# Kernel tuning notes

Hardware: AMD Instinct MI355X
Metric: run time of the kernel (lower is better)

Reference implementation:

```python
import jax, jax.numpy as jnp
import numpy as np

TEMP_LEN = 16
TARGET_LEN = 22
DIM = 768
HEADS = 12
B = 16
NT = TEMP_LEN * TEMP_LEN          # 256 template tokens
NG = TARGET_LEN * TARGET_LEN      # 484 target tokens
N = NT + NG                       # 740
POS_HID = 512


def _gaussian_heatmap(center, size, sig=1.0):
    x_axis = np.linspace(0, size[0] - 1, size[0]) - center[0]
    y_axis = np.linspace(0, size[1] - 1, size[1]) - center[1]
    xx, yy = np.meshgrid(x_axis, y_axis)
    return np.exp(-0.5 * (xx ** 2 + yy ** 2) / sig ** 2)


def _bias_index(L):
    # faithful to getBiasIndex (w_len == h_len here)
    coords = np.stack(np.meshgrid(np.arange(L), np.arange(L), indexing='ij'))  # [2,L,L]
    flat = coords.reshape(2, -1)                                               # [2,L*L]
    rel = (flat[:, :, None] - flat[:, None, :]).transpose(1, 2, 0).astype(np.int64)
    rel[:, :, 0] += L - 1
    rel[:, :, 1] += L - 1
    rel[:, :, 0] *= 2 * L - 1
    return rel.sum(-1)  # [L*L, L*L]


def setup_inputs() -> dict:
    key = jax.random.key(0)
    ks = jax.random.split(key, 12)
    f32 = jnp.float32
    x = jax.random.normal(ks[0], (B, N, DIM), dtype=f32)
    temp_q = jax.random.normal(ks[1], (B, NT, DIM), dtype=f32)
    target_q = jax.random.normal(ks[2], (B, NG, DIM), dtype=f32)
    # linear weights stored [in, out] (transposed torch layout)
    w = lambda k, i, o: jax.random.normal(k, (i, o), dtype=f32) * 0.02
    q_w = w(ks[3], DIM, DIM)
    k_w = w(ks[4], DIM, DIM)
    v_w = w(ks[5], DIM, DIM)
    proj_w = w(ks[6], DIM, DIM)
    proj_b = jnp.zeros((DIM,), dtype=f32)
    rpb_table = jax.random.normal(ks[7], ((2 * TARGET_LEN - 1) ** 2, HEADS), dtype=f32) * 0.0002
    rpb_table_temp = jax.random.normal(ks[8], ((2 * TEMP_LEN - 1) ** 2, HEADS), dtype=f32) * 0.0002
    pos_w1 = w(ks[9], 2, POS_HID)
    pos_b1 = jnp.zeros((POS_HID,), dtype=f32)
    pos_w2 = w(ks[10], POS_HID, HEADS)
    pos_b2 = jnp.zeros((HEADS,), dtype=f32)
    # deterministic cross-bias coordinate table (non-learned buffer)
    temp_tab = _gaussian_heatmap((TEMP_LEN // 2, TEMP_LEN // 2), (TEMP_LEN, TEMP_LEN)).astype(np.float32).flatten() \
        + np.linspace(-0.2, 0.2, NT, dtype=np.float32)
    targ_tab = _gaussian_heatmap((TARGET_LEN // 2, TARGET_LEN // 2), (TARGET_LEN, TARGET_LEN)).astype(np.float32).flatten() \
        + np.linspace(-0.2, 0.2, NG, dtype=np.float32)
    # torch.meshgrid default indexing='ij': [2, NT, NG] -> permute(1,2,0) -> [NT,NG,2]
    temp_target = np.stack(np.meshgrid(temp_tab, targ_tab, indexing='ij')).transpose(1, 2, 0)
    target_temp_tab = jnp.asarray(temp_target.transpose(1, 0, 2))  # [NG, NT, 2]
    temp_idx = jnp.asarray(_bias_index(TEMP_LEN))       # [NT, NT] int64
    target_idx = jnp.asarray(_bias_index(TARGET_LEN))   # [NG, NG] int64
    return {
        'x': x, 'temp_q': temp_q, 'target_q': target_q,
        'q_w': q_w, 'k_w': k_w, 'v_w': v_w, 'proj_w': proj_w, 'proj_b': proj_b,
        'rpb_table': rpb_table, 'rpb_table_temp': rpb_table_temp,
        'pos_w1': pos_w1, 'pos_b1': pos_b1, 'pos_w2': pos_w2, 'pos_b2': pos_b2,
        'target_temp_tab': target_temp_tab,
        'temp_idx': temp_idx, 'target_idx': target_idx,
    }


def reference(x, temp_q, target_q, q_w, k_w, v_w, proj_w, proj_b,
              rpb_table, rpb_table_temp, pos_w1, pos_b1, pos_w2, pos_b2,
              target_temp_tab, temp_idx, target_idx):
    Bsz, Ntok, C = x.shape
    H = HEADS
    hd = C // H
    scale = hd ** -0.5

    q_in = jnp.concatenate([temp_q, target_q], axis=1)                 # [B,N,C]
    q = (q_in @ q_w).reshape(Bsz, Ntok, H, hd).transpose(0, 2, 1, 3)   # [B,H,N,hd]
    k = (x @ k_w).reshape(Bsz, Ntok, H, hd).transpose(0, 2, 1, 3)
    v = (x @ v_w).reshape(Bsz, Ntok, H, hd).transpose(0, 2, 1, 3)

    # gathered relative position biases -> [H, Ni, Ni]
    temp_rpb = rpb_table_temp[temp_idx.reshape(-1)].reshape(NT, NT, H).transpose(2, 0, 1)
    targ_rpb = rpb_table[target_idx.reshape(-1)].reshape(NG, NG, H).transpose(2, 0, 1)
    # MLP cross bias: [NG, NT, 2] -> [NG, NT, H] -> [H, NG, NT]
    hid = jax.nn.relu(target_temp_tab @ pos_w1 + pos_b1)
    target_temp_bias = (hid @ pos_w2 + pos_b2).transpose(2, 0, 1)      # [H,NG,NT]
    temp_target_bias = target_temp_bias.transpose(0, 2, 1)             # [H,NT,NG]
    top = jnp.concatenate([temp_rpb, temp_target_bias], axis=2)        # [H,NT,N]
    bot = jnp.concatenate([target_temp_bias, targ_rpb], axis=2)        # [H,NG,N]
    bias = jnp.concatenate([top, bot], axis=1)[None]                   # [1,H,N,N]

    attn = jnp.einsum('bhnd,bhmd->bhnm', q, k) * scale + bias
    attn = jax.nn.softmax(attn, axis=-1)
    out = jnp.einsum('bhnm,bhmd->bhnd', attn, v).transpose(0, 2, 1, 3).reshape(Bsz, Ntok, C)
    return out @ proj_w + proj_b
```

## Files before the change

### kernel.cpp

```cpp
#include <hip/hip_runtime.h>


typedef unsigned short u16;
typedef short bf16x8 __attribute__((ext_vector_type(8)));
typedef float f32x4 __attribute__((ext_vector_type(4)));

#define BSZ   16
#define NTOK  740
#define NTMP  256
#define NTGT  484
#define DIMC  768
#define NHEAD 12
#define HDIM  64
#define MROWS (BSZ*NTOK)
#define LOG2E 1.44269504f
#define NEGS  (-23.0831032f)

__device__ __forceinline__ float bflo(unsigned int u) {
    return __uint_as_float(u << 16);
}
__device__ __forceinline__ float bfhi(unsigned int u) {
    return __uint_as_float(u & 0xffff0000u);
}
__device__ __forceinline__ u16 f2bf(float f) {
    unsigned int u = __float_as_uint(f);
    u += 0x7fffu + ((u >> 16) & 1u);
    return (u16)(u >> 16);
}

__device__ __forceinline__ void gl_lds16(const u16* g, u16* l) {
    __builtin_amdgcn_global_load_lds(
        (const __attribute__((address_space(1))) unsigned int*)(unsigned long long)g,
        (__attribute__((address_space(3))) unsigned int*)(unsigned int)(unsigned long long)l,
        16, 0, 0);
}

__device__ __forceinline__ size_t b2off(int h, int i, int j) {
    return ((size_t)(h * NTOK + i)) * 768 + ((j >> 6) << 6) + ((j & 15) << 2) + ((j >> 4) & 3);
}

#define PREP_MLP  484
#define PREP_TRW  (PREP_MLP + 576)
#define PREP_ALL  (PREP_TRW + 2220)

__global__ __launch_bounds__(256) void prep_kernel(
    const float* __restrict__ w0, const float* __restrict__ w1,
    const float* __restrict__ w2, const float* __restrict__ w3,
    u16* __restrict__ Wt,
    const float* __restrict__ rpb, const float* __restrict__ rpbt,
    const int* __restrict__ tidx, const int* __restrict__ gidx,
    const float* __restrict__ pw1, const float* __restrict__ pb1,
    const float* __restrict__ pw2, const float* __restrict__ pb2,
    const float* __restrict__ tab, u16* __restrict__ bias)
{
    __shared__ float T[64][65];
    const int blk = blockIdx.x;
    const int tid = threadIdx.x;

    if (blk < PREP_MLP) {
        int g = blk;
        int t = tid;
        float a  = tab[(g * NTMP + t) * 2 + 0];
        float bb = tab[(g * NTMP + t) * 2 + 1];
        float acc[NHEAD];
        #pragma unroll
        for (int h = 0; h < NHEAD; h++) acc[h] = pb2[h];
        for (int k = 0; k < 512; k++) {
            float hid = fmaxf(a * pw1[k] + bb * pw1[512 + k] + pb1[k], 0.0f);
            #pragma unroll
            for (int h = 0; h < NHEAD; h++) acc[h] += hid * pw2[k * NHEAD + h];
        }
        #pragma unroll
        for (int h = 0; h < NHEAD; h++) {
            u16 v = f2bf(acc[h] * LOG2E);
            bias[b2off(h, t, NTMP + g)] = v;
            bias[b2off(h, NTMP + g, t)] = v;
        }
    } else if (blk < PREP_TRW) {
        int t = blk - PREP_MLP;
        int z = t / 144, rem = t - z * 144;
        int bx = rem % 12, by = rem / 12;
        const float* src = (z == 0) ? w0 : (z == 1) ? w1 : (z == 2) ? w2 : w3;
        const float scale = (z == 0) ? 0.125f * LOG2E : 1.0f;
        u16* dst = Wt + (size_t)z * DIMC * DIMC;
        int out0 = bx * 64, in0 = by * 64;
        #pragma unroll
        for (int l = 0; l < 4; l++) {
            int u = tid + (l << 8);
            int r = u >> 4, c4 = (u & 15) << 2;
            float4 p = *(const float4*)(src + (size_t)(in0 + r) * DIMC + out0 + c4);
            T[r][c4] = p.x; T[r][c4 + 1] = p.y; T[r][c4 + 2] = p.z; T[r][c4 + 3] = p.w;
        }
        __syncthreads();
        #pragma unroll
        for (int l = 0; l < 2; l++) {
            int u = tid + (l << 8);
            int r = u >> 3, c8 = (u & 7) << 3;
            u16 e[8];
            #pragma unroll
            for (int i = 0; i < 8; i++) e[i] = f2bf(T[c8 + i][r] * scale);
            *(uint4*)(dst + (size_t)(out0 + r) * DIMC + in0 + c8) = *(uint4*)e;
        }
    } else {
        int t = blk - PREP_TRW;
        int jb = t % 3, i = t / 3;
        int j = jb * 256 + tid;
        u16 vals[NHEAD];
        if (j >= NTOK) {
            u16 neg = f2bf(-1e30f);
            #pragma unroll
            for (int h = 0; h < NHEAD; h++) vals[h] = neg;
        } else if (i < NTMP && j < NTMP) {
            int idx = tidx[i * NTMP + j];
            #pragma unroll
            for (int h = 0; h < NHEAD; h++) vals[h] = f2bf(rpbt[idx * NHEAD + h] * LOG2E);
        } else if (i >= NTMP && j >= NTMP) {
            int idx = gidx[(i - NTMP) * NTGT + (j - NTMP)];
            #pragma unroll
            for (int h = 0; h < NHEAD; h++) vals[h] = f2bf(rpb[idx * NHEAD + h] * LOG2E);
        } else {
            return;
        }
        #pragma unroll
        for (int h = 0; h < NHEAD; h++) bias[b2off(h, i, j)] = vals[h];
    }
}

__global__ __launch_bounds__(256, 6) void gemm_qkv(
    const float* __restrict__ x, const float* __restrict__ tq,
    const float* __restrict__ gq, const u16* __restrict__ Wt,
    u16* __restrict__ Qo, u16* __restrict__ Ko, u16* __restrict__ Vo)
{
    __shared__ __align__(16) u16 As[4096];
    __shared__ __align__(16) u16 Bs[8192];
    const int tid = threadIdx.x;
    const int lane = tid & 63, w = tid >> 6;
    const int quad = lane >> 4, ln = lane & 15;

    const int nwg = 18 * 185;
    const int flat = blockIdx.y * 18 + blockIdx.x;
    const int q = nwg >> 3, r = nwg & 7;
    const int xcd = flat & 7, sidx = flat >> 3;
    const int wg = (xcd < r) ? xcd * (q + 1) + sidx
                             : r * (q + 1) + (xcd - r) * q + sidx;
    const int by = wg / 18, bx = wg - by * 18;

    const int m0 = by << 6;
    const int wm = (w >> 1) << 5, wn = (w & 1) << 6;

    const int p = (bx < 6) ? 0 : (bx < 12) ? 1 : 2;
    const int nn = (bx - p * 6) << 7;
    const u16* Wb = Wt + (size_t)p * DIMC * DIMC + (size_t)nn * DIMC;
    u16* Co = (p == 0) ? Qo : (p == 1) ? Ko : Vo;

    const int rr = tid >> 2, qq = tid & 3;
    const int arow = m0 + rr;
    const float* aptr;
    if (p == 0) {
        int b = arow / NTOK, n = arow - b * NTOK;
        aptr = (n < NTMP)
             ? tq + ((size_t)(b * NTMP + n)) * DIMC
             : gq + ((size_t)(b * NTGT + (n - NTMP))) * DIMC;
    } else {
        aptr = x + (size_t)arow * DIMC;
    }
    const int wof0 = ((2 * qq + 0) * 64 + (rr ^ (2 * qq + 0))) * 8;
    const int wof1 = ((2 * qq + 1) * 64 + (rr ^ (2 * qq + 1))) * 8;

    f32x4 acc[2][4];
    #pragma unroll
    for (int i = 0; i < 2; i++)
        #pragma unroll
        for (int j = 0; j < 4; j++) acc[i][j] = (f32x4){0.f, 0.f, 0.f, 0.f};

    #pragma unroll 1
    for (int t = 0; t < 12; t++) {
        const int k0 = t << 6;
        __syncthreads();
        const float* s = aptr + k0 + (qq << 4);
        float4 a0 = ((const float4*)s)[0], a1 = ((const float4*)s)[1];
        float4 a2 = ((const float4*)s)[2], a3 = ((const float4*)s)[3];
        #pragma unroll
        for (int l = 0; l < 4; l++) {
            int f = tid + (l << 8);
            int c8 = f >> 7, r2 = f & 127;
            gl_lds16(Wb + (size_t)r2 * DIMC + k0 + c8 * 8, &Bs[f * 8]);
        }
        u16 e[16] = {f2bf(a0.x), f2bf(a0.y), f2bf(a0.z), f2bf(a0.w),
                     f2bf(a1.x), f2bf(a1.y), f2bf(a1.z), f2bf(a1.w),
                     f2bf(a2.x), f2bf(a2.y), f2bf(a2.z), f2bf(a2.w),
                     f2bf(a3.x), f2bf(a3.y), f2bf(a3.z), f2bf(a3.w)};
        *(uint4*)&As[wof0] = ((uint4*)e)[0];
        *(uint4*)&As[wof1] = ((uint4*)e)[1];
        __syncthreads();
        #pragma unroll
        for (int kp = 0; kp < 2; kp++) {
            const int kc0 = (kp << 2) + quad;
            bf16x8 af[2], bfr[4];
            #pragma unroll
            for (int mt = 0; mt < 2; mt++)
                af[mt] = *(const bf16x8*)
                    &As[(kc0 * 64 + wm + mt * 16 + (ln ^ kc0)) * 8];
            #pragma unroll
            for (int nt = 0; nt < 4; nt++)
                bfr[nt] = *(const bf16x8*)
                    &Bs[(kc0 * 128 + wn + nt * 16 + ln) * 8];
            #pragma unroll
            for (int mt = 0; mt < 2; mt++)
                #pragma unroll
                for (int nt = 0; nt < 4; nt++)
                    acc[mt][nt] = __builtin_amdgcn_mfma_f32_16x16x32_bf16(
                        af[mt], bfr[nt], acc[mt][nt], 0, 0, 0);
        }
    }

    #pragma unroll
    for (int mt = 0; mt < 2; mt++)
        #pragma unroll
        for (int reg = 0; reg < 4; reg++) {
            int grow = m0 + wm + mt * 16 + (quad << 2) + reg;
            #pragma unroll
            for (int nt = 0; nt < 4; nt++)
                Co[(size_t)grow * DIMC + nn + wn + nt * 16 + ln]
                    = f2bf(acc[mt][nt][reg]);
        }
}

__global__ __launch_bounds__(256) void gemm_proj(
    const u16* __restrict__ A, const u16* __restrict__ Wt,
    const float* __restrict__ pb, float* __restrict__ Cf)
{
    __shared__ __align__(16) u16 As[4096];
    __shared__ __align__(16) u16 Bs[8192];
    const int tid = threadIdx.x;
    const int lane = tid & 63, w = tid >> 6;
    const int quad = lane >> 4, ln = lane & 15;

    const int nwg = 6 * 185;
    const int flat = blockIdx.y * 6 + blockIdx.x;
    const int q = nwg >> 3, r = nwg & 7;
    const int xcd = flat & 7, sidx = flat >> 3;
    const int wg = (xcd < r) ? xcd * (q + 1) + sidx
                             : r * (q + 1) + (xcd - r) * q + sidx;
    const int by = wg / 6, bx = wg - by * 6;

    const int m0 = by << 6;
    const int wm = (w >> 1) << 5, wn = (w & 1) << 6;
    const int nn = bx << 7;
    const u16* Wb = Wt + (size_t)nn * DIMC;

    f32x4 acc[2][4];
    #pragma unroll
    for (int i = 0; i < 2; i++)
        #pragma unroll
        for (int j = 0; j < 4; j++) acc[i][j] = (f32x4){0.f, 0.f, 0.f, 0.f};

    #pragma unroll 1
    for (int t = 0; t < 12; t++) {
        __syncthreads();
        const int k0 = t << 6;
        #pragma unroll
        for (int l = 0; l < 2; l++) {
            int f = tid + (l << 8);
            int c8 = f >> 6, r2 = f & 63;
            gl_lds16(A + (size_t)(m0 + r2) * DIMC + k0 + c8 * 8, &As[f * 8]);
        }
        #pragma unroll
        for (int l = 0; l < 4; l++) {
            int f = tid + (l << 8);
            int c8 = f >> 7, r2 = f & 127;
            gl_lds16(Wb + (size_t)r2 * DIMC + k0 + c8 * 8, &Bs[f * 8]);
        }
        __syncthreads();
        #pragma unroll
        for (int kp = 0; kp < 2; kp++) {
            bf16x8 af[2], bfr[4];
            #pragma unroll
            for (int mt = 0; mt < 2; mt++)
                af[mt] = *(const bf16x8*)
                    &As[(((kp << 2) + quad) * 64 + wm + mt * 16 + ln) * 8];
            #pragma unroll
            for (int nt = 0; nt < 4; nt++)
                bfr[nt] = *(const bf16x8*)
                    &Bs[(((kp << 2) + quad) * 128 + wn + nt * 16 + ln) * 8];
            #pragma unroll
            for (int mt = 0; mt < 2; mt++)
                #pragma unroll
                for (int nt = 0; nt < 4; nt++)
                    acc[mt][nt] = __builtin_amdgcn_mfma_f32_16x16x32_bf16(
                        af[mt], bfr[nt], acc[mt][nt], 0, 0, 0);
        }
    }

    #pragma unroll
    for (int mt = 0; mt < 2; mt++)
        #pragma unroll
        for (int reg = 0; reg < 4; reg++) {
            int grow = m0 + wm + mt * 16 + (quad << 2) + reg;
            #pragma unroll
            for (int nt = 0; nt < 4; nt++) {
                int gcol = nn + wn + nt * 16 + ln;
                Cf[(size_t)grow * DIMC + gcol] = acc[mt][nt][reg] + pb[gcol];
            }
        }
}

__global__ __launch_bounds__(256) void attn_mfma(
    const u16* __restrict__ Qg, const u16* __restrict__ Kg,
    const u16* __restrict__ Vg, const u16* __restrict__ bias,
    u16* __restrict__ ctx)
{
    __shared__ __align__(16) u16 KsL[4096];
    __shared__ __align__(16) u16 VtL[64 * 72];
    __shared__ __align__(16) u16 Pw[4][16][72];

    const int tid = threadIdx.x;
    const int lane = tid & 63, w = tid >> 6;
    const int quad = lane >> 4, ln = lane & 15;

    const int flat = (blockIdx.z * 12 + blockIdx.y) * 12 + blockIdx.x;
    const int wg = (flat & 7) * 288 + (flat >> 3);
    const int h = wg / 192;
    const int rem = wg - h * 192;
    const int b = rem / 12;
    const int q0 = (rem - b * 12) << 6;

    const int mbase = q0 + (w << 4);
    const u16* bp = bias + ((size_t)h * NTOK) * 768;

    bf16x8 aq[2];
    {
        int qrow = mbase + ln; if (qrow >= NTOK) qrow = NTOK - 1;
        #pragma unroll
        for (int kp = 0; kp < 2; kp++)
            aq[kp] = *(const bf16x8*)(Qg + ((size_t)(b * NTOK + qrow)) * DIMC
                                      + h * HDIM + kp * 32 + (quad << 3));
    }
    int boff[4];
    #pragma unroll
    for (int reg = 0; reg < 4; reg++) {
        int rr = mbase + (quad << 2) + reg;
        if (rr >= NTOK) rr = NTOK - 1;
        boff[reg] = rr * 768 + (ln << 2);
    }

    const int pswz = ((ln >> 2) & 3) << 4;

    float rs[4] = {};
    f32x4 O[4];
    #pragma unroll
    for (int dt = 0; dt < 4; dt++) O[dt] = (f32x4){0.f, 0.f, 0.f, 0.f};

    for (int j0 = 0; j0 < NTOK; j0 += 64) {
        __syncthreads();
        #pragma unroll
        for (int l = 0; l < 2; l++) {
            int f = tid + (l << 8);
            int chunk = f >> 6, jr = f & 63;
            int krow = j0 + jr; if (krow >= NTOK) krow = NTOK - 1;
            gl_lds16(Kg + ((size_t)(b * NTOK + krow)) * DIMC + h * HDIM + chunk * 8,
                     KsL + f * 8);
        }
        uint2 bvv[4];
        #pragma unroll
        for (int reg = 0; reg < 4; reg++)
            bvv[reg] = *(const uint2*)(bp + boff[reg] + j0);
        #pragma unroll
        for (int l = 0; l < 2; l++) {
            int u = tid + (l << 8);
            int jr = u >> 3, d0 = (u & 7) << 3;
            int vrow = j0 + jr; if (vrow >= NTOK) vrow = NTOK - 1;
            uint4 p = *(const uint4*)(Vg + ((size_t)(b * NTOK + vrow)) * DIMC + h * HDIM + d0);
            const u16* pe = (const u16*)&p;
            int jswz = jr ^ d0;
            #pragma unroll
            for (int i = 0; i < 8; i++) VtL[(d0 + i) * 72 + jswz] = pe[i];
        }
        __syncthreads();

        bf16x8 bv[4][2];
        #pragma unroll
        for (int dt = 0; dt < 4; dt++) {
            int key8 = ((dt * 2 + (ln >> 3)) & 7) << 3;
            #pragma unroll
            for (int kp = 0; kp < 2; kp++) {
                int koff = (kp * 32 + (quad << 3)) ^ key8;
                bv[dt][kp] = *(const bf16x8*)&VtL[(dt * 16 + ln) * 72 + koff];
            }
        }

        f32x4 s[4];
        #pragma unroll
        for (int nt = 0; nt < 4; nt++) s[nt] = (f32x4){NEGS, NEGS, NEGS, NEGS};
        __builtin_amdgcn_s_setprio(1);
        #pragma unroll
        for (int kp = 0; kp < 2; kp++)
            #pragma unroll
            for (int nt = 0; nt < 4; nt++) {
                bf16x8 bk = *(const bf16x8*)
                    &KsL[(((kp << 2) + quad) * 64 + nt * 16 + ln) * 8];
                s[nt] = __builtin_amdgcn_mfma_f32_16x16x32_bf16(aq[kp], bk, s[nt], 0, 0, 0);
            }
        __builtin_amdgcn_s_setprio(0);

        #pragma unroll
        for (int reg = 0; reg < 4; reg++) {
            uint2 bb = bvv[reg];
            float p0 = __builtin_exp2f(s[0][reg] + bflo(bb.x));
            float p1 = __builtin_exp2f(s[1][reg] + bfhi(bb.x));
            float p2 = __builtin_exp2f(s[2][reg] + bflo(bb.y));
            float p3 = __builtin_exp2f(s[3][reg] + bfhi(bb.y));
            s[0][reg] = p0; s[1][reg] = p1;
            s[2][reg] = p2; s[3][reg] = p3;
            rs[reg] += p0 + p1 + p2 + p3;
        }
        u16* pwb = &Pw[w][0][0];
        #pragma unroll
        for (int nt = 0; nt < 4; nt++) {
            int colw = ((nt ^ quad) << 4) + ln;
            #pragma unroll
            for (int reg = 0; reg < 4; reg++)
                pwb[((quad << 2) + reg) * 72 + colw] = f2bf(s[nt][reg]);
        }
        bf16x8 ap[2];
        #pragma unroll
        for (int kp = 0; kp < 2; kp++) {
            int koff = (kp * 32 + (quad << 3)) ^ pswz;
            ap[kp] = *(const bf16x8*)&pwb[ln * 72 + koff];
        }
        __builtin_amdgcn_s_setprio(1);
        #pragma unroll
        for (int dt = 0; dt < 4; dt++)
            #pragma unroll
            for (int kp = 0; kp < 2; kp++)
                O[dt] = __builtin_amdgcn_mfma_f32_16x16x32_bf16(
                    ap[kp], bv[dt][kp], O[dt], 0, 0, 0);
        __builtin_amdgcn_s_setprio(0);
    }

    #pragma unroll
    for (int reg = 0; reg < 4; reg++) {
        float t = rs[reg];
        #pragma unroll
        for (int mk = 8; mk >= 1; mk >>= 1) t += __shfl_xor(t, mk);
        float inv = 1.0f / t;
        int row = mbase + (quad << 2) + reg;
        if (row < NTOK) {
            #pragma unroll
            for (int dt = 0; dt < 4; dt++)
                ctx[((size_t)(b * NTOK + row)) * DIMC + h * HDIM + dt * 16 + ln]
                    = f2bf(O[dt][reg] * inv);
        }
    }
}

extern "C" void kernel_launch(void* const* d_in, const int* in_sizes, int n_in,
                              void* d_out, int out_size, void* d_ws, size_t ws_size,
                              hipStream_t stream)
{
    const float* x        = (const float*)d_in[0];
    const float* temp_q   = (const float*)d_in[1];
    const float* target_q = (const float*)d_in[2];
    const float* q_w      = (const float*)d_in[3];
    const float* k_w      = (const float*)d_in[4];
    const float* v_w      = (const float*)d_in[5];
    const float* proj_w   = (const float*)d_in[6];
    const float* proj_b   = (const float*)d_in[7];
    const float* rpb      = (const float*)d_in[8];
    const float* rpbt     = (const float*)d_in[9];
    const float* pw1      = (const float*)d_in[10];
    const float* pb1      = (const float*)d_in[11];
    const float* pw2      = (const float*)d_in[12];
    const float* pb2      = (const float*)d_in[13];
    const float* tab      = (const float*)d_in[14];
    const int*   tidx     = (const int*)d_in[15];
    const int*   gidx     = (const int*)d_in[16];
    float* out = (float*)d_out;

    char* ws = (char*)d_ws;
    const size_t S = (size_t)MROWS * DIMC * sizeof(u16);
    const size_t SZB = (size_t)NHEAD * NTOK * 768 * sizeof(u16);
    u16* CTX   = (u16*)(ws);
    u16* V     = (u16*)(ws + S);
    u16* Q     = (u16*)(ws + 2 * S);
    u16* K     = (u16*)(ws + 3 * S);
    u16* BIAS2 = (u16*)(ws + 4 * S);
    u16* WT    = (u16*)(ws + 4 * S + SZB);

    prep_kernel<<<dim3(PREP_ALL), 256, 0, stream>>>(
        q_w, k_w, v_w, proj_w, WT,
        rpb, rpbt, tidx, gidx,
        pw1, pb1, pw2, pb2, tab, BIAS2);

    const u16* WTp = WT + 3 * (size_t)DIMC * DIMC;

    gemm_qkv<<<dim3(18, 185), 256, 0, stream>>>(x, temp_q, target_q, WT, Q, K, V);
    attn_mfma<<<dim3(12, 12, 16), 256, 0, stream>>>(Q, K, V, BIAS2, CTX);
    gemm_proj<<<dim3(6, 185), 256, 0, stream>>>(CTX, WTp, proj_b, out);
}
```

Measured before the change: 470.7 us.

## Keep A rows resident in QKV GEMM and double-buffer attention K/V/bias loads

The QKV GEMM now runs one 512-thread block per 64-row strip (Q strip or shared K/V strip). Each block converts the full fp32 A rows to bf16 into LDS once and loops over all output column tiles, with a double-buffered weight stage. This removes the repeated fp32 A reads and bf16 conversions across the 18 column blocks. In exchange, only 370 large blocks are launched, with heavy LDS use and uneven work between Q and K/V blocks, so occupancy and load balance may suffer. The attention kernel also double-buffers K in LDS and prefetches the next V and bias tiles into registers to overlap global loads with MFMA work.

```diff
diff --git a/kernel.cpp b/kernel.cpp
--- a/kernel.cpp
+++ b/kernel.cpp
@@ -126,104 +126,124 @@
     }
 }
 
-__global__ __launch_bounds__(256, 6) void gemm_qkv(
+__global__ __launch_bounds__(512) void gemm_qkv(
     const float* __restrict__ x, const float* __restrict__ tq,
     const float* __restrict__ gq, const u16* __restrict__ Wt,
     u16* __restrict__ Qo, u16* __restrict__ Ko, u16* __restrict__ Vo)
 {
-    __shared__ __align__(16) u16 As[4096];
-    __shared__ __align__(16) u16 Bs[8192];
+    __shared__ __align__(16) u16 As[96 * 64 * 8];
+    __shared__ __align__(16) u16 Bs[2][8192];
     const int tid = threadIdx.x;
     const int lane = tid & 63, w = tid >> 6;
     const int quad = lane >> 4, ln = lane & 15;
 
-    const int nwg = 18 * 185;
-    const int flat = blockIdx.y * 18 + blockIdx.x;
+    const int nwg = 370;
+    const int flat = blockIdx.x;
     const int q = nwg >> 3, r = nwg & 7;
     const int xcd = flat & 7, sidx = flat >> 3;
     const int wg = (xcd < r) ? xcd * (q + 1) + sidx
                              : r * (q + 1) + (xcd - r) * q + sidx;
-    const int by = wg / 18, bx = wg - by * 18;
-
+    const int kvtype = (wg >= 185) ? 1 : 0;
+    const int by = kvtype ? (wg - 185) : wg;
     const int m0 = by << 6;
-    const int wm = (w >> 1) << 5, wn = (w & 1) << 6;
-
-    const int p = (bx < 6) ? 0 : (bx < 12) ? 1 : 2;
-    const int nn = (bx - p * 6) << 7;
-    const u16* Wb = Wt + (size_t)p * DIMC * DIMC + (size_t)nn * DIMC;
-    u16* Co = (p == 0) ? Qo : (p == 1) ? Ko : Vo;
-
-    const int rr = tid >> 2, qq = tid & 3;
+
+    const int wm = (w >> 2) << 5;
+    const int wn = (w & 3) << 5;
+
+    const int rr = tid >> 3, qe = tid & 7;
     const int arow = m0 + rr;
     const float* aptr;
-    if (p == 0) {
+    if (!kvtype) {
         int b = arow / NTOK, n = arow - b * NTOK;
-        aptr = (n < NTMP)
-             ? tq + ((size_t)(b * NTMP + n)) * DIMC
-             : gq + ((size_t)(b * NTGT + (n - NTMP))) * DIMC;
+        aptr = (n < NTMP) ? tq + ((size_t)(b * NTMP + n)) * DIMC
+                          : gq + ((size_t)(b * NTGT + (n - NTMP))) * DIMC;
     } else {
         aptr = x + (size_t)arow * DIMC;
     }
-    const int wof0 = ((2 * qq + 0) * 64 + (rr ^ (2 * qq + 0))) * 8;
-    const int wof1 = ((2 * qq + 1) * 64 + (rr ^ (2 * qq + 1))) * 8;
-
-    f32x4 acc[2][4];
-    #pragma unroll
-    for (int i = 0; i < 2; i++)
-        #pragma unroll
-        for (int j = 0; j < 4; j++) acc[i][j] = (f32x4){0.f, 0.f, 0.f, 0.f};
-
-    #pragma unroll 1
-    for (int t = 0; t < 12; t++) {
-        const int k0 = t << 6;
-        __syncthreads();
-        const float* s = aptr + k0 + (qq << 4);
+    #pragma unroll
+    for (int j = 0; j < 12; j++) {
+        const float* s = aptr + j * 64 + qe * 8;
         float4 a0 = ((const float4*)s)[0], a1 = ((const float4*)s)[1];
-        float4 a2 = ((const float4*)s)[2], a3 = ((const float4*)s)[3];
-        #pragma unroll
-        for (int l = 0; l < 4; l++) {
-            int f = tid + (l << 8);
-            int c8 = f >> 7, r2 = f & 127;
-            gl_lds16(Wb + (size_t)r2 * DIMC + k0 + c8 * 8, &Bs[f * 8]);
-        }
-        u16 e[16] = {f2bf(a0.x), f2bf(a0.y), f2bf(a0.z), f2bf(a0.w),
-                     f2bf(a1.x), f2bf(a1.y), f2bf(a1.z), f2bf(a1.w),
-                     f2bf(a2.x), f2bf(a2.y), f2bf(a2.z), f2bf(a2.w),
-                     f2bf(a3.x), f2bf(a3.y), f2bf(a3.z), f2bf(a3.w)};
-        *(uint4*)&As[wof0] = ((uint4*)e)[0];
-        *(uint4*)&As[wof1] = ((uint4*)e)[1];
-        __syncthreads();
-        #pragma unroll
-        for (int kp = 0; kp < 2; kp++) {
-            const int kc0 = (kp << 2) + quad;
-            bf16x8 af[2], bfr[4];
-            #pragma unroll
-            for (int mt = 0; mt < 2; mt++)
-                af[mt] = *(const bf16x8*)
-                    &As[(kc0 * 64 + wm + mt * 16 + (ln ^ kc0)) * 8];
-            #pragma unroll
-            for (int nt = 0; nt < 4; nt++)
-                bfr[nt] = *(const bf16x8*)
-                    &Bs[(kc0 * 128 + wn + nt * 16 + ln) * 8];
-            #pragma unroll
-            for (int mt = 0; mt < 2; mt++)
+        u16 e[8] = {f2bf(a0.x), f2bf(a0.y), f2bf(a0.z), f2bf(a0.w),
+                    f2bf(a1.x), f2bf(a1.y), f2bf(a1.z), f2bf(a1.w)};
+        *(uint4*)&As[((j * 8 + qe) * 64 + (rr ^ qe)) * 8] = *(uint4*)e;
+    }
+
+#define WB_OF(pi) ((!kvtype) ? (Wt + ((size_t)(pi) << 7) * DIMC)                          \
+                 : ((pi) < 6) ? (Wt + (size_t)DIMC * DIMC + ((size_t)(pi) << 7) * DIMC)   \
+                              : (Wt + 2 * (size_t)DIMC * DIMC + ((size_t)((pi) - 6) << 7) * DIMC))
+
+#define STAGEB(Wb, t, s) do {                                                 \
+    _Pragma("unroll")                                                         \
+    for (int l = 0; l < 2; l++) {                                             \
+        int f = tid + (l << 9);                                               \
+        int c8 = f >> 7, r2 = f & 127;                                        \
+        gl_lds16((Wb) + (size_t)r2 * DIMC + ((t) << 6) + c8 * 8,              \
+                 &Bs[s][f * 8]);                                              \
+    } } while (0)
+
+    const int NP = kvtype ? 12 : 6;
+    STAGEB(WB_OF(0), 0, 0);
+    __syncthreads();
+
+    int buf = 0;
+    for (int pi = 0; pi < NP; pi++) {
+        const u16* WbC = WB_OF(pi);
+        const u16* WbN = (pi + 1 < NP) ? WB_OF(pi + 1) : WbC;
+        f32x4 acc[2][2];
+        #pragma unroll
+        for (int i = 0; i < 2; i++)
+            #pragma unroll
+            for (int j = 0; j < 2; j++) acc[i][j] = (f32x4){0.f, 0.f, 0.f, 0.f};
+
+        #pragma unroll 1
+        for (int t = 0; t < 12; t++) {
+            if (!((pi == NP - 1) && (t == 11))) {
+                const u16* Ws = (t < 11) ? WbC : WbN;
+                int tn = (t < 11) ? (t + 1) : 0;
+                STAGEB(Ws, tn, buf ^ 1);
+            }
+            #pragma unroll
+            for (int kp = 0; kp < 2; kp++) {
+                const int key = (kp << 2) + quad;
+                const int C = (t << 3) + key;
+                bf16x8 af[2], bfr[2];
                 #pragma unroll
-                for (int nt = 0; nt < 4; nt++)
-                    acc[mt][nt] = __builtin_amdgcn_mfma_f32_16x16x32_bf16(
-                        af[mt], bfr[nt], acc[mt][nt], 0, 0, 0);
-        }
-    }
-
-    #pragma unroll
-    for (int mt = 0; mt < 2; mt++)
-        #pragma unroll
-        for (int reg = 0; reg < 4; reg++) {
-            int grow = m0 + wm + mt * 16 + (quad << 2) + reg;
-            #pragma unroll
-            for (int nt = 0; nt < 4; nt++)
-                Co[(size_t)grow * DIMC + nn + wn + nt * 16 + ln]
-                    = f2bf(acc[mt][nt][reg]);
-        }
+                for (int mt = 0; mt < 2; mt++)
+                    af[mt] = *(const bf16x8*)
+                        &As[(C * 64 + ((wm + mt * 16 + ln) ^ key)) * 8];
+                #pragma unroll
+                for (int nt = 0; nt < 2; nt++)
+                    bfr[nt] = *(const bf16x8*)
+                        &Bs[buf][(key * 128 + wn + nt * 16 + ln) * 8];
+                #pragma unroll
+                for (int mt = 0; mt < 2; mt++)
+                    #pragma unroll
+                    for (int nt = 0; nt < 2; nt++)
+                        acc[mt][nt] = __builtin_amdgcn_mfma_f32_16x16x32_bf16(
+                            af[mt], bfr[nt], acc[mt][nt], 0, 0, 0);
+            }
+            __syncthreads();
+            buf ^= 1;
+        }
+
+        u16* Co; int nn;
+        if (!kvtype)      { Co = Qo; nn = pi << 7; }
+        else if (pi < 6)  { Co = Ko; nn = pi << 7; }
+        else              { Co = Vo; nn = (pi - 6) << 7; }
+        #pragma unroll
+        for (int mt = 0; mt < 2; mt++)
+            #pragma unroll
+            for (int reg = 0; reg < 4; reg++) {
+                int grow = m0 + wm + mt * 16 + (quad << 2) + reg;
+                #pragma unroll
+                for (int nt = 0; nt < 2; nt++)
+                    Co[(size_t)grow * DIMC + nn + wn + nt * 16 + ln]
+                        = f2bf(acc[mt][nt][reg]);
+            }
+    }
+#undef WB_OF
+#undef STAGEB
 }
 
 __global__ __launch_bounds__(256) void gemm_proj(
@@ -310,7 +330,7 @@
     const u16* __restrict__ Vg, const u16* __restrict__ bias,
     u16* __restrict__ ctx)
 {
-    __shared__ __align__(16) u16 KsL[4096];
+    __shared__ __align__(16) u16 KsL[2][4096];
     __shared__ __align__(16) u16 VtL[64 * 72];
     __shared__ __align__(16) u16 Pw[4][16][72];
 
@@ -344,6 +364,13 @@
         boff[reg] = rr * 768 + (ln << 2);
     }
 
+    int vjr[2], vd0[2];
+    #pragma unroll
+    for (int l = 0; l < 2; l++) {
+        int u = tid + (l << 8);
+        vjr[l] = u >> 3; vd0[l] = (u & 7) << 3;
+    }
+
     const int pswz = ((ln >> 2) & 3) << 4;
 
     float rs[4] = {};
@@ -351,32 +378,58 @@
     #pragma unroll
     for (int dt = 0; dt < 4; dt++) O[dt] = (f32x4){0.f, 0.f, 0.f, 0.f};
 
-    for (int j0 = 0; j0 < NTOK; j0 += 64) {
-        __syncthreads();
-        #pragma unroll
-        for (int l = 0; l < 2; l++) {
-            int f = tid + (l << 8);
-            int chunk = f >> 6, jr = f & 63;
-            int krow = j0 + jr; if (krow >= NTOK) krow = NTOK - 1;
-            gl_lds16(Kg + ((size_t)(b * NTOK + krow)) * DIMC + h * HDIM + chunk * 8,
-                     KsL + f * 8);
-        }
-        uint2 bvv[4];
-        #pragma unroll
-        for (int reg = 0; reg < 4; reg++)
-            bvv[reg] = *(const uint2*)(bp + boff[reg] + j0);
-        #pragma unroll
-        for (int l = 0; l < 2; l++) {
-            int u = tid + (l << 8);
-            int jr = u >> 3, d0 = (u & 7) << 3;
-            int vrow = j0 + jr; if (vrow >= NTOK) vrow = NTOK - 1;
-            uint4 p = *(const uint4*)(Vg + ((size_t)(b * NTOK + vrow)) * DIMC + h * HDIM + d0);
-            const u16* pe = (const u16*)&p;
-            int jswz = jr ^ d0;
-            #pragma unroll
-            for (int i = 0; i < 8; i++) VtL[(d0 + i) * 72 + jswz] = pe[i];
-        }
-        __syncthreads();
+    uint4 vp[2];
+    uint2 bvv[4], bvn[4];
+
+#define STAGE_K(j0, s) do {                                                   \
+    _Pragma("unroll")                                                         \
+    for (int l = 0; l < 2; l++) {                                             \
+        int f = tid + (l << 8);                                               \
+        int chunk = f >> 6, jr = f & 63;                                      \
+        int krow = (j0) + jr; if (krow >= NTOK) krow = NTOK - 1;              \
+        gl_lds16(Kg + ((size_t)(b * NTOK + krow)) * DIMC + h * HDIM + chunk * 8, \
+                 &KsL[s][f * 8]);                                             \
+    } } while (0)
+
+#define LOAD_V(j0, dst) do {                                                  \
+    _Pragma("unroll")                                                         \
+    for (int l = 0; l < 2; l++) {                                             \
+        int vrow = (j0) + vjr[l]; if (vrow >= NTOK) vrow = NTOK - 1;          \
+        dst[l] = *(const uint4*)(Vg + ((size_t)(b * NTOK + vrow)) * DIMC      \
+                                 + h * HDIM + vd0[l]);                        \
+    } } while (0)
+
+#define WRITE_V(src) do {                                                     \
+    _Pragma("unroll")                                                         \
+    for (int l = 0; l < 2; l++) {                                             \
+        const u16* pe = (const u16*)&src[l];                                  \
+        int jswz = vjr[l] ^ vd0[l];                                           \
+        _Pragma("unroll")                                                     \
+        for (int i = 0; i < 8; i++)                                           \
+            VtL[(vd0[l] + i) * 72 + jswz] = pe[i];                            \
+    } } while (0)
+
+#define LOAD_B(j0, dst) do {                                                  \
+    _Pragma("unroll")                                                         \
+    for (int reg = 0; reg < 4; reg++)                                         \
+        dst[reg] = *(const uint2*)(bp + boff[reg] + (j0));                    \
+    } while (0)
+
+    STAGE_K(0, 0);
+    LOAD_V(0, vp);
+    LOAD_B(0, bvv);
+    __syncthreads();
+    WRITE_V(vp);
+    __syncthreads();
+
+    for (int tt = 0; tt < 12; tt++) {
+        const int p = tt & 1;
+        if (tt < 11) {
+            const int j0n = (tt + 1) << 6;
+            STAGE_K(j0n, p ^ 1);
+            LOAD_V(j0n, vp);
+            LOAD_B(j0n, bvn);
+        }
 
         bf16x8 bv[4][2];
         #pragma unroll
@@ -398,7 +451,7 @@
             #pragma unroll
             for (int nt = 0; nt < 4; nt++) {
                 bf16x8 bk = *(const bf16x8*)
-                    &KsL[(((kp << 2) + quad) * 64 + nt * 16 + ln) * 8];
+                    &KsL[p][(((kp << 2) + quad) * 64 + nt * 16 + ln) * 8];
                 s[nt] = __builtin_amdgcn_mfma_f32_16x16x32_bf16(aq[kp], bk, s[nt], 0, 0, 0);
             }
         __builtin_amdgcn_s_setprio(0);
@@ -436,7 +489,20 @@
                 O[dt] = __builtin_amdgcn_mfma_f32_16x16x32_bf16(
                     ap[kp], bv[dt][kp], O[dt], 0, 0, 0);
         __builtin_amdgcn_s_setprio(0);
-    }
+
+        __syncthreads();
+        if (tt < 11) {
+            WRITE_V(vp);
+            #pragma unroll
+            for (int reg = 0; reg < 4; reg++) bvv[reg] = bvn[reg];
+            __syncthreads();
+        }
+    }
+
+#undef STAGE_K
+#undef LOAD_V
+#undef WRITE_V
+#undef LOAD_B
 
     #pragma unroll
     for (int reg = 0; reg < 4; reg++) {
@@ -494,7 +560,7 @@
 
     const u16* WTp = WT + 3 * (size_t)DIMC * DIMC;
 
-    gemm_qkv<<<dim3(18, 185), 256, 0, stream>>>(x, temp_q, target_q, WT, Q, K, V);
+    gemm_qkv<<<dim3(370), 512, 0, stream>>>(x, temp_q, target_q, WT, Q, K, V);
     attn_mfma<<<dim3(12, 12, 16), 256, 0, stream>>>(Q, K, V, BIAS2, CTX);
     gemm_proj<<<dim3(6, 185), 256, 0, stream>>>(CTX, WTp, proj_b, out);
 }
```

After: 598.9 us. 1.27x slower.

## Double-buffer QKV and projection GEMMs and enlarge projection tile to 128x128

Applied to the files above, without the earlier changes.

Both GEMMs now prefetch the next k-slice while computing the current one. QKV prefetches A into registers and B into a second LDS buffer; the projection double-buffers A and B in LDS. The projection GEMM uses 128x128 tiles with a 4x4 MFMA accumulator per wave and a halved grid, with clamped loads and guarded stores for the partial last row tile. This aims to hide global load latency and increase reuse, at the cost of more LDS and registers, and lower occupancy in the QKV kernel.

```diff
diff --git a/kernel.cpp b/kernel.cpp
--- a/kernel.cpp
+++ b/kernel.cpp
@@ -126,13 +126,13 @@
     }
 }
 
-__global__ __launch_bounds__(256, 6) void gemm_qkv(
+__global__ __launch_bounds__(256, 4) void gemm_qkv(
     const float* __restrict__ x, const float* __restrict__ tq,
     const float* __restrict__ gq, const u16* __restrict__ Wt,
     u16* __restrict__ Qo, u16* __restrict__ Ko, u16* __restrict__ Vo)
 {
     __shared__ __align__(16) u16 As[4096];
-    __shared__ __align__(16) u16 Bs[8192];
+    __shared__ __align__(16) u16 Bs[2][8192];
     const int tid = threadIdx.x;
     const int lane = tid & 63, w = tid >> 6;
     const int quad = lane >> 4, ln = lane & 15;
@@ -167,32 +167,50 @@
     const int wof0 = ((2 * qq + 0) * 64 + (rr ^ (2 * qq + 0))) * 8;
     const int wof1 = ((2 * qq + 1) * 64 + (rr ^ (2 * qq + 1))) * 8;
 
+    float4 a0, a1, a2, a3;
+
+#define LOADA(t) do {                                                         \
+    const float* s_ = aptr + ((t) << 6) + (qq << 4);                          \
+    a0 = ((const float4*)s_)[0]; a1 = ((const float4*)s_)[1];                 \
+    a2 = ((const float4*)s_)[2]; a3 = ((const float4*)s_)[3];                 \
+    } while (0)
+
+#define WRITEA() do {                                                         \
+    u16 e_[16] = {f2bf(a0.x), f2bf(a0.y), f2bf(a0.z), f2bf(a0.w),             \
+                  f2bf(a1.x), f2bf(a1.y), f2bf(a1.z), f2bf(a1.w),             \
+                  f2bf(a2.x), f2bf(a2.y), f2bf(a2.z), f2bf(a2.w),             \
+                  f2bf(a3.x), f2bf(a3.y), f2bf(a3.z), f2bf(a3.w)};            \
+    *(uint4*)&As[wof0] = ((uint4*)e_)[0];                                     \
+    *(uint4*)&As[wof1] = ((uint4*)e_)[1];                                     \
+    } while (0)
+
+#define STAGEB(t, s) do {                                                     \
+    _Pragma("unroll")                                                         \
+    for (int l = 0; l < 4; l++) {                                             \
+        int f = tid + (l << 8);                                               \
+        int c8 = f >> 7, r2 = f & 127;                                        \
+        gl_lds16(Wb + (size_t)r2 * DIMC + ((t) << 6) + c8 * 8, &Bs[s][f * 8]); \
+    } } while (0)
+
     f32x4 acc[2][4];
     #pragma unroll
     for (int i = 0; i < 2; i++)
         #pragma unroll
         for (int j = 0; j < 4; j++) acc[i][j] = (f32x4){0.f, 0.f, 0.f, 0.f};
 
+    LOADA(0);
+    STAGEB(0, 0);
+    __syncthreads();
+    WRITEA();
+    __syncthreads();
+
+    int buf = 0;
     #pragma unroll 1
     for (int t = 0; t < 12; t++) {
-        const int k0 = t << 6;
-        __syncthreads();
-        const float* s = aptr + k0 + (qq << 4);
-        float4 a0 = ((const float4*)s)[0], a1 = ((const float4*)s)[1];
-        float4 a2 = ((const float4*)s)[2], a3 = ((const float4*)s)[3];
-        #pragma unroll
-        for (int l = 0; l < 4; l++) {
-            int f = tid + (l << 8);
-            int c8 = f >> 7, r2 = f & 127;
-            gl_lds16(Wb + (size_t)r2 * DIMC + k0 + c8 * 8, &Bs[f * 8]);
-        }
-        u16 e[16] = {f2bf(a0.x), f2bf(a0.y), f2bf(a0.z), f2bf(a0.w),
-                     f2bf(a1.x), f2bf(a1.y), f2bf(a1.z), f2bf(a1.w),
-                     f2bf(a2.x), f2bf(a2.y), f2bf(a2.z), f2bf(a2.w),
-                     f2bf(a3.x), f2bf(a3.y), f2bf(a3.z), f2bf(a3.w)};
-        *(uint4*)&As[wof0] = ((uint4*)e)[0];
-        *(uint4*)&As[wof1] = ((uint4*)e)[1];
-        __syncthreads();
+        if (t < 11) {
+            LOADA(t + 1);
+            STAGEB(t + 1, buf ^ 1);
+        }
         #pragma unroll
         for (int kp = 0; kp < 2; kp++) {
             const int kc0 = (kp << 2) + quad;
@@ -200,11 +218,11 @@
             #pragma unroll
             for (int mt = 0; mt < 2; mt++)
                 af[mt] = *(const bf16x8*)
-                    &As[(kc0 * 64 + wm + mt * 16 + (ln ^ kc0)) * 8];
+                    &As[(kc0 * 64 + ((wm + mt * 16 + ln) ^ kc0)) * 8];
             #pragma unroll
             for (int nt = 0; nt < 4; nt++)
                 bfr[nt] = *(const bf16x8*)
-                    &Bs[(kc0 * 128 + wn + nt * 16 + ln) * 8];
+                    &Bs[buf][(kc0 * 128 + wn + nt * 16 + ln) * 8];
             #pragma unroll
             for (int mt = 0; mt < 2; mt++)
                 #pragma unroll
@@ -212,7 +230,16 @@
                     acc[mt][nt] = __builtin_amdgcn_mfma_f32_16x16x32_bf16(
                         af[mt], bfr[nt], acc[mt][nt], 0, 0, 0);
         }
-    }
+        if (t < 11) {
+            __syncthreads();
+            WRITEA();
+            __syncthreads();
+            buf ^= 1;
+        }
+    }
+#undef LOADA
+#undef WRITEA
+#undef STAGEB
 
     #pragma unroll
     for (int mt = 0; mt < 2; mt++)
@@ -230,13 +257,13 @@
     const u16* __restrict__ A, const u16* __restrict__ Wt,
     const float* __restrict__ pb, float* __restrict__ Cf)
 {
-    __shared__ __align__(16) u16 As[4096];
-    __shared__ __align__(16) u16 Bs[8192];
+    __shared__ __align__(16) u16 As[2][8192];
+    __shared__ __align__(16) u16 Bs[2][8192];
     const int tid = threadIdx.x;
     const int lane = tid & 63, w = tid >> 6;
     const int quad = lane >> 4, ln = lane & 15;
 
-    const int nwg = 6 * 185;
+    const int nwg = 6 * 93;
     const int flat = blockIdx.y * 6 + blockIdx.x;
     const int q = nwg >> 3, r = nwg & 7;
     const int xcd = flat & 7, sidx = flat >> 3;
@@ -244,65 +271,76 @@
                              : r * (q + 1) + (xcd - r) * q + sidx;
     const int by = wg / 6, bx = wg - by * 6;
 
-    const int m0 = by << 6;
-    const int wm = (w >> 1) << 5, wn = (w & 1) << 6;
+    const int m0 = by << 7;
+    const int wm = (w >> 1) << 6, wn = (w & 1) << 6;
     const int nn = bx << 7;
     const u16* Wb = Wt + (size_t)nn * DIMC;
 
-    f32x4 acc[2][4];
-    #pragma unroll
-    for (int i = 0; i < 2; i++)
-        #pragma unroll
-        for (int j = 0; j < 4; j++) acc[i][j] = (f32x4){0.f, 0.f, 0.f, 0.f};
-
+    f32x4 acc[4][4];
+    #pragma unroll
+    for (int i = 0; i < 4; i++)
+        #pragma unroll
+        for (int j = 0; j < 4; j++)
+            acc[i][j] = (f32x4){0.f, 0.f, 0.f, 0.f};
+
+#define STAGE(s, k0) do {                                                     \
+    _Pragma("unroll")                                                         \
+    for (int l = 0; l < 4; l++) {                                             \
+        int f = tid + (l << 8);                                  \
+        int c8 = f >> 7, rr = f & 127;                                        \
+        int grow = m0 + rr; if (grow >= MROWS) grow = MROWS - 1;              \
+        gl_lds16(A + (size_t)grow * DIMC + (k0) + c8 * 8, &As[s][f * 8]);     \
+        gl_lds16(Wb + (size_t)rr * DIMC + (k0) + c8 * 8, &Bs[s][f * 8]);      \
+    } } while (0)
+
+#define COMPUTE(s) do {                                                       \
+    _Pragma("unroll")                                                         \
+    for (int kp = 0; kp < 2; kp++) {                                          \
+        bf16x8 af[4], bfr[4];                                                 \
+        _Pragma("unroll")                                                     \
+        for (int mt = 0; mt < 4; mt++)                                        \
+            af[mt] = *(const bf16x8*)                                         \
+                &As[s][(((kp << 2) + quad) * 128 + wm + mt * 16 + ln) * 8];   \
+        _Pragma("unroll")                                                     \
+        for (int nt = 0; nt < 4; nt++)                                        \
+            bfr[nt] = *(const bf16x8*)                                        \
+                &Bs[s][(((kp << 2) + quad) * 128 + wn + nt * 16 + ln) * 8];   \
+        _Pragma("unroll")                                                     \
+        for (int mt = 0; mt < 4; mt++)                                        \
+            _Pragma("unroll")                                                 \
+            for (int nt = 0; nt < 4; nt++)                                    \
+                acc[mt][nt] = __builtin_amdgcn_mfma_f32_16x16x32_bf16(        \
+                    af[mt], bfr[nt], acc[mt][nt], 0, 0, 0);                   \
+    } } while (0)
+
+    STAGE(0, 0);
+    __syncthreads();
     #pragma unroll 1
-    for (int t = 0; t < 12; t++) {
+    for (int t = 0; t < 12; t += 2) {
+        STAGE(1, (t + 1) << 6);
+        COMPUTE(0);
         __syncthreads();
-        const int k0 = t << 6;
-        #pragma unroll
-        for (int l = 0; l < 2; l++) {
-            int f = tid + (l << 8);
-            int c8 = f >> 6, r2 = f & 63;
-            gl_lds16(A + (size_t)(m0 + r2) * DIMC + k0 + c8 * 8, &As[f * 8]);
-        }
-        #pragma unroll
-        for (int l = 0; l < 4; l++) {
-            int f = tid + (l << 8);
-            int c8 = f >> 7, r2 = f & 127;
-            gl_lds16(Wb + (size_t)r2 * DIMC + k0 + c8 * 8, &Bs[f * 8]);
-        }
+        if (t < 10) STAGE(0, (t + 2) << 6);
+        COMPUTE(1);
         __syncthreads();
-        #pragma unroll
-        for (int kp = 0; kp < 2; kp++) {
-            bf16x8 af[2], bfr[4];
-            #pragma unroll
-            for (int mt = 0; mt < 2; mt++)
-                af[mt] = *(const bf16x8*)
-                    &As[(((kp << 2) + quad) * 64 + wm + mt * 16 + ln) * 8];
-            #pragma unroll
-            for (int nt = 0; nt < 4; nt++)
-                bfr[nt] = *(const bf16x8*)
-                    &Bs[(((kp << 2) + quad) * 128 + wn + nt * 16 + ln) * 8];
-            #pragma unroll
-            for (int mt = 0; mt < 2; mt++)
-                #pragma unroll
-                for (int nt = 0; nt < 4; nt++)
-                    acc[mt][nt] = __builtin_amdgcn_mfma_f32_16x16x32_bf16(
-                        af[mt], bfr[nt], acc[mt][nt], 0, 0, 0);
-        }
-    }
-
-    #pragma unroll
-    for (int mt = 0; mt < 2; mt++)
+    }
+
+#undef STAGE
+#undef COMPUTE
+
+    #pragma unroll
+    for (int mt = 0; mt < 4; mt++) {
         #pragma unroll
         for (int reg = 0; reg < 4; reg++) {
             int grow = m0 + wm + mt * 16 + (quad << 2) + reg;
+            if (grow >= MROWS) continue;
             #pragma unroll
             for (int nt = 0; nt < 4; nt++) {
                 int gcol = nn + wn + nt * 16 + ln;
                 Cf[(size_t)grow * DIMC + gcol] = acc[mt][nt][reg] + pb[gcol];
             }
         }
+    }
 }
 
 __global__ __launch_bounds__(256) void attn_mfma(
@@ -496,5 +534,5 @@
 
     gemm_qkv<<<dim3(18, 185), 256, 0, stream>>>(x, temp_q, target_q, WT, Q, K, V);
     attn_mfma<<<dim3(12, 12, 16), 256, 0, stream>>>(Q, K, V, BIAS2, CTX);
-    gemm_proj<<<dim3(6, 185), 256, 0, stream>>>(CTX, WTp, proj_b, out);
-}
+    gemm_proj<<<dim3(6, 93), 256, 0, stream>>>(CTX, WTp, proj_b, out);
+}
```

Result: no change. 472.8 us (+0.4%).
